# Kernel tuning notes

Hardware: AMD Instinct MI355X
Metric: run time of the kernel (lower is better)

Reference implementation:

```python
import jax, jax.numpy as jnp
import numpy as np

G = 3  # group_num
EPS = 1e-5


def _ln(x, g, b):
    m = x.mean(-1, keepdims=True)
    v = x.var(-1, keepdims=True)
    return (x - m) / jnp.sqrt(v + EPS) * g + b


def _gcm(x, w_qk, b_qk, ct_w1, ct_b1, ct_g, ct_be, ct_w2, ct_b2,
         lw_w1, lw_b1, lw_g, lw_be, lw_w2, lw_b2):
    # x: [B, 768, H, W] (pre-concatenated group feature)
    b, c, h, w = x.shape
    gc = c // G
    # channel shuffle: b (g c) h w -> b (c g) h w
    xs = x.reshape(b, G, gc, h, w).transpose(0, 2, 1, 3, 4).reshape(b, c, h, w)
    out = xs.reshape(b, G, gc, h, w)            # b g c h w
    value = out.reshape(b, G, gc, h * w)        # b g c n
    # fc_qk (Linear gc->1) over the channel axis, softmax over spatial n
    logits = jnp.einsum('bgcn,c->bgn', value, w_qk) + b_qk
    attn = jax.nn.softmax(logits, axis=-1)       # b g n
    context = jnp.einsum('bgcn,bgn->bgc', value, attn)  # b g c
    lvl_context = context.reshape(b, c)          # b (g c)
    # ctx_transform: Linear -> LN -> ReLU -> Linear
    h1 = jax.nn.relu(_ln(context @ ct_w1.T + ct_b1, ct_g, ct_be))
    ctx = h1 @ ct_w2.T + ct_b2                   # b g c
    # lvl_weight: Linear -> LN -> ReLU -> Linear -> Sigmoid
    l1 = jax.nn.relu(_ln(lvl_context @ lw_w1.T + lw_b1, lw_g, lw_be))
    lvlw = jax.nn.sigmoid(l1 @ lw_w2.T + lw_b2)  # b g (=3)
    ctx = ctx * lvlw[:, :, None]
    return (out + ctx[:, :, :, None, None]).sum(axis=1)  # b c_g h w


def setup_inputs() -> dict:
    key = jax.random.key(0)
    ks = jax.random.split(key, 16)
    B = 8
    sizes = [(128, 128), (64, 64), (32, 32), (16, 16)]
    inp = {}
    for i, (h, w) in enumerate(sizes):
        inp[f'g{i}'] = jax.random.normal(ks[i], (B, 768, h, w), jnp.float32)
    inp['x_last'] = jax.random.normal(ks[4], (B, 256, 8, 8), jnp.float32)
    s = 0.05
    inp['w_qk'] = jax.random.normal(ks[5], (4, 256), jnp.float32) * s
    inp['b_qk'] = jax.random.normal(ks[6], (4,), jnp.float32) * s
    inp['ct_w1'] = jax.random.normal(ks[7], (4, 64, 256), jnp.float32) * s
    inp['ct_b1'] = jax.random.normal(ks[8], (4, 64), jnp.float32) * s
    inp['ct_g'] = jnp.ones((4, 64), jnp.float32)
    inp['ct_be'] = jnp.zeros((4, 64), jnp.float32)
    inp['ct_w2'] = jax.random.normal(ks[9], (4, 256, 64), jnp.float32) * s
    inp['ct_b2'] = jax.random.normal(ks[10], (4, 256), jnp.float32) * s
    inp['lw_w1'] = jax.random.normal(ks[11], (4, 768, 768), jnp.float32) * s
    inp['lw_b1'] = jax.random.normal(ks[12], (4, 768), jnp.float32) * s
    inp['lw_g'] = jnp.ones((4, 768), jnp.float32)
    inp['lw_be'] = jnp.zeros((4, 768), jnp.float32)
    inp['lw_w2'] = jax.random.normal(ks[13], (4, 3, 768), jnp.float32) * s
    inp['lw_b2'] = jax.random.normal(ks[14], (4, 3), jnp.float32) * s
    return inp


def reference(g0, g1, g2, g3, x_last, w_qk, b_qk, ct_w1, ct_b1, ct_g, ct_be,
              ct_w2, ct_b2, lw_w1, lw_b1, lw_g, lw_be, lw_w2, lw_b2):
    outs = []
    for i, g in enumerate([g0, g1, g2, g3]):
        outs.append(_gcm(g, w_qk[i], b_qk[i], ct_w1[i], ct_b1[i], ct_g[i],
                         ct_be[i], ct_w2[i], ct_b2[i], lw_w1[i], lw_b1[i],
                         lw_g[i], lw_be[i], lw_w2[i], lw_b2[i]))
    return (*outs, x_last)
```

## Files before the change

### kernel.cpp

```cpp
#include <hip/hip_runtime.h>

#define NB 8
#define NWG 680
#define PSTRIDE 772

typedef float f4 __attribute__((ext_vector_type(4)));

__device__ __forceinline__ f4 ntload(const float* p) {
  return __builtin_nontemporal_load((const f4*)p);
}
__device__ __forceinline__ void ntstore(float* p, f4 v) {
  __builtin_nontemporal_store(v, (f4*)p);
}
__device__ __forceinline__ float hsum(f4 v) { return v.x + v.y + v.z + v.w; }

struct KFArgs {
  const float* x[4];
  float* outp[4];
  float* partial;
  int N[4];
};

__global__ __launch_bounds__(512, 2) void kf_fused(KFArgs a, const float* __restrict__ wqk_all) {
  __shared__ float red[2][768];
  __shared__ float zl[24];

  int wg = blockIdx.x;
  int lvl, b, idx;
  if (wg < 512)      { lvl = 0; b = wg >> 6;            idx = wg & 63; }
  else if (wg < 640) { int r = wg - 512; lvl = 1; b = r >> 4; idx = r & 15; }
  else if (wg < 672) { int r = wg - 640; lvl = 2; b = r >> 2; idx = r & 3; }
  else               { int r = wg - 672; lvl = 3; b = r;      idx = 0; }
  int N = a.N[lvl];
  int col0 = idx * 256;
  const float* __restrict__ xb = a.x[lvl] + (size_t)b * 768 * N;
  float* __restrict__ outb = a.outp[lvl] + (size_t)b * 256 * N;
  int tid = threadIdx.x;
  int snq = tid & 7, oq = tid >> 3, wv = tid >> 6;

  int srow[4][3];
  float wq[4];
#pragma unroll
  for (int j = 0; j < 4; ++j) {
    int c2 = oq + 64 * j;
    wq[j] = wqk_all[lvl * 256 + c2];
#pragma unroll
    for (int k = 0; k < 3; ++k) {
      int f = c2 + (k << 8);
      srow[j][k] = (f % 3) * 256 + f / 3;
    }
  }

  float acc[4][3] = {{0.f, 0.f, 0.f}, {0.f, 0.f, 0.f}, {0.f, 0.f, 0.f}, {0.f, 0.f, 0.f}};
  float za[3] = {0.f, 0.f, 0.f};

  f4 A[12], B[12];

  auto issue = [&](f4* buf, int tile) {
    int n0 = col0 + tile * 32 + snq * 4;
#pragma unroll
    for (int j = 0; j < 4; ++j)
#pragma unroll
      for (int k = 0; k < 3; ++k)
        buf[j * 3 + k] = ntload(xb + (size_t)srow[j][k] * N + n0);
  };

  auto body = [&](f4* cur, f4* nxt, int tt, bool pre) {
    int n0 = col0 + tt * 32 + snq * 4;
    if (pre) issue(nxt, tt + 1);
    f4 pg[3] = {{0.f, 0.f, 0.f, 0.f}, {0.f, 0.f, 0.f, 0.f}, {0.f, 0.f, 0.f, 0.f}};
#pragma unroll
    for (int j = 0; j < 4; ++j)
#pragma unroll
      for (int k = 0; k < 3; ++k)
        pg[k] += cur[j * 3 + k] * wq[j];
#pragma unroll
    for (int k = 0; k < 3; ++k) {
#pragma unroll
      for (int m = 8; m <= 32; m <<= 1) {
        pg[k].x += __shfl_xor(pg[k].x, m);
        pg[k].y += __shfl_xor(pg[k].y, m);
        pg[k].z += __shfl_xor(pg[k].z, m);
        pg[k].w += __shfl_xor(pg[k].w, m);
      }
    }
    float* rb = red[tt & 1];
    if ((tid & 63) < 8) {
#pragma unroll
      for (int k = 0; k < 3; ++k)
        *(f4*)(rb + (wv * 24 + k * 8 + snq) * 4) = pg[k];
    }
    asm volatile("s_waitcnt lgkmcnt(0)" ::: "memory");
    __builtin_amdgcn_sched_barrier(0);
    __builtin_amdgcn_s_barrier();
    __builtin_amdgcn_sched_barrier(0);
    f4 sev[3];
#pragma unroll
    for (int k = 0; k < 3; ++k) {
      f4 s = {0.f, 0.f, 0.f, 0.f};
#pragma unroll
      for (int w = 0; w < 8; ++w) s += *(const f4*)(rb + (w * 24 + k * 8 + snq) * 4);
      f4 e;
      e.x = __expf(s.x); e.y = __expf(s.y); e.z = __expf(s.z); e.w = __expf(s.w);
      sev[k] = e;
    }
    if (tid < 8) {
#pragma unroll
      for (int k = 0; k < 3; ++k) za[k] += hsum(sev[k]);
    }
#pragma unroll
    for (int j = 0; j < 4; ++j) {
      f4 ov = cur[j * 3 + 0] + cur[j * 3 + 1] + cur[j * 3 + 2];
      *(f4*)(outb + (size_t)(oq + 64 * j) * N + n0) = ov;
#pragma unroll
      for (int k = 0; k < 3; ++k)
        acc[j][k] += hsum(cur[j * 3 + k] * sev[k]);
    }
  };

  issue(A, 0);
  for (int tt = 0; tt < 8; tt += 2) {
    body(A, B, tt, true);
    body(B, A, tt + 1, tt + 1 < 7);
  }

  float* pw = a.partial + (size_t)wg * PSTRIDE;
#pragma unroll
  for (int j = 0; j < 4; ++j)
#pragma unroll
    for (int k = 0; k < 3; ++k) {
      float v = acc[j][k];
      v += __shfl_xor(v, 1);
      v += __shfl_xor(v, 2);
      v += __shfl_xor(v, 4);
      if (snq == 0) pw[k * 256 + oq + 64 * j] = v;
    }
  if (tid < 8) {
#pragma unroll
    for (int k = 0; k < 3; ++k) zl[tid * 3 + k] = za[k];
  }
  __syncthreads();
  if (tid < 3) {
    float z = 0.f;
#pragma unroll
    for (int s = 0; s < 8; ++s) z += zl[s * 3 + tid];
    pw[768 + tid] = z;
  }
}

__device__ __forceinline__ float blk_sum256(float v, float* sr4) {
  for (int o = 32; o; o >>= 1) v += __shfl_xor(v, o);
  __syncthreads();
  if ((threadIdx.x & 63) == 0) sr4[threadIdx.x >> 6] = v;
  __syncthreads();
  return sr4[0] + sr4[1] + sr4[2] + sr4[3];
}

__global__ __launch_bounds__(256) void k4_mlp(
    const float* __restrict__ partial,
    const float* __restrict__ ct_w1, const float* __restrict__ ct_b1,
    const float* __restrict__ ct_g,  const float* __restrict__ ct_be,
    const float* __restrict__ ct_w2, const float* __restrict__ ct_b2,
    const float* __restrict__ lw_w1, const float* __restrict__ lw_b1,
    const float* __restrict__ lw_g,  const float* __restrict__ lw_be,
    const float* __restrict__ lw_w2, const float* __restrict__ lw_b2,
    float* __restrict__ add_all) {
  int b = blockIdx.x, lvl = blockIdx.y;
  int t = threadIdx.x;
  static const int cnt_[4] = {64, 16, 4, 1};
  static const int base_[4] = {0, 512, 640, 672};
  int cnt = cnt_[lvl];
  int wg0 = base_[lvl] + b * cnt;

  const float* w1 = ct_w1 + lvl * 64 * 256;
  const float* b1 = ct_b1 + lvl * 64;
  const float* cg = ct_g + lvl * 64;
  const float* cbe = ct_be + lvl * 64;
  const float* w2 = ct_w2 + lvl * 256 * 64;
  const float* b2 = ct_b2 + lvl * 256;
  const float* W1 = lw_w1 + (size_t)lvl * 768 * 768;
  const float* B1 = lw_b1 + lvl * 768;
  const float* Lg = lw_g + lvl * 768;
  const float* Lbe = lw_be + lvl * 768;
  const float* W2 = lw_w2 + lvl * 3 * 768;
  const float* B2 = lw_b2 + lvl * 3;
  float* addp = add_all + ((size_t)lvl * NB + b) * 256;

  __shared__ float sctx[768];
  __shared__ float sh1[3][64];
  __shared__ float sl1[768];
  __shared__ float slvlw[3];
  __shared__ float sr4[4];
  __shared__ float sZ[3];

  float s0 = 0.f, s1 = 0.f, s2 = 0.f;
  for (int w = 0; w < cnt; ++w) {
    const float* pw = partial + (size_t)(wg0 + w) * PSTRIDE;
    s0 += pw[t];
    s1 += pw[t + 256];
    s2 += pw[t + 512];
  }
  if (t < 3) {
    float z = 0.f;
    for (int w = 0; w < cnt; ++w) z += partial[(size_t)(wg0 + w) * PSTRIDE + 768 + t];
    sZ[t] = z;
  }
  __syncthreads();
  sctx[t] = s0 / sZ[0];
  sctx[t + 256] = s1 / sZ[1];
  sctx[t + 512] = s2 / sZ[2];
  __syncthreads();

  if (t < 192) {
    int g = t >> 6, j = t & 63;
    const f4* w4 = (const f4*)(w1 + j * 256);
    const f4* c4 = (const f4*)(sctx + g * 256);
    f4 acc = {0.f, 0.f, 0.f, 0.f};
#pragma unroll 8
    for (int k = 0; k < 64; ++k) acc += c4[k] * w4[k];
    sh1[g][j] = hsum(acc) + b1[j];
  }
  __syncthreads();
  int wv = t >> 6, ln = t & 63;
  if (wv < 3) {
    float v = sh1[wv][ln];
    float s = v;
    for (int o = 32; o; o >>= 1) s += __shfl_xor(s, o);
    float mean = s * (1.f / 64.f);
    float d = v - mean;
    float q = d * d;
    for (int o = 32; o; o >>= 1) q += __shfl_xor(q, o);
    float var = q * (1.f / 64.f);
    float y = d * rsqrtf(var + 1e-5f) * cg[ln] + cbe[ln];
    sh1[wv][ln] = fmaxf(y, 0.f);
  }
  __syncthreads();
  float l1v[3];
#pragma unroll
  for (int r = 0; r < 3; ++r) {
    int j = t + r * 256;
    const f4* W4 = (const f4*)(W1 + (size_t)j * 768);
    const f4* s4 = (const f4*)sctx;
    f4 acc = {0.f, 0.f, 0.f, 0.f};
#pragma unroll 8
    for (int k = 0; k < 192; ++k) acc += s4[k] * W4[k];
    l1v[r] = hsum(acc) + B1[j];
  }
  float S = blk_sum256(l1v[0] + l1v[1] + l1v[2], sr4);
  float mean = S * (1.f / 768.f);
  float q = 0.f;
#pragma unroll
  for (int r = 0; r < 3; ++r) { float d = l1v[r] - mean; q += d * d; }
  float var = blk_sum256(q, sr4) * (1.f / 768.f);
  float inv = rsqrtf(var + 1e-5f);
#pragma unroll
  for (int r = 0; r < 3; ++r) {
    int j = t + r * 256;
    float y = (l1v[r] - mean) * inv * Lg[j] + Lbe[j];
    sl1[j] = fmaxf(y, 0.f);
  }
  __syncthreads();
  if (wv < 3) {
    float acc = 0.f;
    for (int j = ln; j < 768; j += 64) acc = fmaf(sl1[j], W2[wv * 768 + j], acc);
    for (int o = 32; o; o >>= 1) acc += __shfl_xor(acc, o);
    if (ln == 0) slvlw[wv] = 1.f / (1.f + __expf(-(acc + B2[wv])));
  }
  __syncthreads();
  {
    int c2 = t;
    float a = 0.f;
#pragma unroll
    for (int g = 0; g < 3; ++g) {
      const f4* w4 = (const f4*)(w2 + c2 * 64);
      const f4* h4 = (const f4*)(sh1[g]);
      f4 acc = {0.f, 0.f, 0.f, 0.f};
#pragma unroll
      for (int j = 0; j < 16; ++j) acc += h4[j] * w4[j];
      a += (hsum(acc) + b2[c2]) * slvlw[g];
    }
    addp[c2] = a;
  }
}

__global__ __launch_bounds__(256) void k5_add(float* __restrict__ out,
                                              const float* __restrict__ add_all,
                                              const float* __restrict__ xlast) {
  size_t f4i = (size_t)blockIdx.x * 256 + threadIdx.x;
  if (f4i >= 11141120) {
    size_t r = f4i - 11141120;
    f4 v = ntload(xlast + (r << 2));
    ntstore(out + (f4i << 2), v);
    return;
  }
  int lvl, lgN2;
  size_t base;
  if (f4i < 8388608)       { lvl = 0; base = 0;        lgN2 = 12; }
  else if (f4i < 10485760) { lvl = 1; base = 8388608;  lgN2 = 10; }
  else if (f4i < 11010048) { lvl = 2; base = 10485760; lgN2 = 8;  }
  else                     { lvl = 3; base = 11010048; lgN2 = 6;  }
  size_t lf4 = f4i - base;
  int bc = (int)(lf4 >> lgN2);
  float a = add_all[lvl * 2048 + bc];
  float* p = out + (f4i << 2);
  f4 v = *(const f4*)p;
  v += a;
  ntstore(p, v);
}

extern "C" void kernel_launch(void* const* d_in, const int* in_sizes, int n_in,
                              void* d_out, int out_size, void* d_ws, size_t ws_size,
                              hipStream_t stream) {
  const float* gx[4] = {(const float*)d_in[0], (const float*)d_in[1],
                        (const float*)d_in[2], (const float*)d_in[3]};
  const float* x_last = (const float*)d_in[4];
  const float* w_qk = (const float*)d_in[5];
  const float* ct_w1 = (const float*)d_in[7];
  const float* ct_b1 = (const float*)d_in[8];
  const float* ct_g  = (const float*)d_in[9];
  const float* ct_be = (const float*)d_in[10];
  const float* ct_w2 = (const float*)d_in[11];
  const float* ct_b2 = (const float*)d_in[12];
  const float* lw_w1 = (const float*)d_in[13];
  const float* lw_b1 = (const float*)d_in[14];
  const float* lw_g  = (const float*)d_in[15];
  const float* lw_be = (const float*)d_in[16];
  const float* lw_w2 = (const float*)d_in[17];
  const float* lw_b2 = (const float*)d_in[18];
  float* out = (float*)d_out;
  float* ws = (float*)d_ws;

  static const int Ns[4] = {16384, 4096, 1024, 256};
  static const size_t outOff[4] = {0, 33554432, 41943040, 44040192};

  float* partb = ws;
  float* addb  = ws + NWG * PSTRIDE;

  KFArgs af;
  for (int i = 0; i < 4; ++i) {
    af.x[i] = gx[i];
    af.outp[i] = out + outOff[i];
    af.N[i] = Ns[i];
  }
  af.partial = partb;

  kf_fused<<<dim3(NWG), dim3(512), 0, stream>>>(af, w_qk);
  k4_mlp<<<dim3(NB, 4), dim3(256), 0, stream>>>(partb, ct_w1, ct_b1, ct_g, ct_be,
                                                ct_w2, ct_b2, lw_w1, lw_b1, lw_g,
                                                lw_be, lw_w2, lw_b2, addb);
  k5_add<<<dim3(43648), dim3(256), 0, stream>>>(out, addb, x_last);
}
```

Baseline: 304.8 us.

## Split fused kernel into one workgroup per 32-column tile, drop software pipelining

Measured after the change: 316.2 us. +3.7%, slower.

```diff
diff --git a/kernel.cpp b/kernel.cpp
--- a/kernel.cpp
+++ b/kernel.cpp
@@ -1,7 +1,7 @@
 #include <hip/hip_runtime.h>
 
 #define NB 8
-#define NWG 680
+#define NTILE 5440
 #define PSTRIDE 772
 
 typedef float f4 __attribute__((ext_vector_type(4)));
@@ -21,22 +21,22 @@
   int N[4];
 };
 
-__global__ __launch_bounds__(512, 2) void kf_fused(KFArgs a, const float* __restrict__ wqk_all) {
-  __shared__ float red[2][768];
+__global__ __launch_bounds__(512, 4) void kf_fused(KFArgs a, const float* __restrict__ wqk_all) {
+  __shared__ float red[768];
   __shared__ float zl[24];
 
   int wg = blockIdx.x;
   int lvl, b, idx;
-  if (wg < 512)      { lvl = 0; b = wg >> 6;            idx = wg & 63; }
-  else if (wg < 640) { int r = wg - 512; lvl = 1; b = r >> 4; idx = r & 15; }
-  else if (wg < 672) { int r = wg - 640; lvl = 2; b = r >> 2; idx = r & 3; }
-  else               { int r = wg - 672; lvl = 3; b = r;      idx = 0; }
+  if (wg < 4096)      { lvl = 0; b = wg >> 9;            idx = wg & 511; }
+  else if (wg < 5120) { int r = wg - 4096; lvl = 1; b = r >> 7; idx = r & 127; }
+  else if (wg < 5376) { int r = wg - 5120; lvl = 2; b = r >> 5; idx = r & 31; }
+  else                { int r = wg - 5376; lvl = 3; b = r >> 3; idx = r & 7; }
   int N = a.N[lvl];
-  int col0 = idx * 256;
   const float* __restrict__ xb = a.x[lvl] + (size_t)b * 768 * N;
   float* __restrict__ outb = a.outp[lvl] + (size_t)b * 256 * N;
   int tid = threadIdx.x;
   int snq = tid & 7, oq = tid >> 3, wv = tid >> 6;
+  int n0 = idx * 32 + snq * 4;
 
   int srow[4][3];
   float wq[4];
@@ -51,77 +51,62 @@
     }
   }
 
-  float acc[4][3] = {{0.f, 0.f, 0.f}, {0.f, 0.f, 0.f}, {0.f, 0.f, 0.f}, {0.f, 0.f, 0.f}};
-  float za[3] = {0.f, 0.f, 0.f};
-
-  f4 A[12], B[12];
-
-  auto issue = [&](f4* buf, int tile) {
-    int n0 = col0 + tile * 32 + snq * 4;
-#pragma unroll
-    for (int j = 0; j < 4; ++j)
-#pragma unroll
-      for (int k = 0; k < 3; ++k)
-        buf[j * 3 + k] = ntload(xb + (size_t)srow[j][k] * N + n0);
-  };
-
-  auto body = [&](f4* cur, f4* nxt, int tt, bool pre) {
-    int n0 = col0 + tt * 32 + snq * 4;
-    if (pre) issue(nxt, tt + 1);
-    f4 pg[3] = {{0.f, 0.f, 0.f, 0.f}, {0.f, 0.f, 0.f, 0.f}, {0.f, 0.f, 0.f, 0.f}};
-#pragma unroll
-    for (int j = 0; j < 4; ++j)
-#pragma unroll
-      for (int k = 0; k < 3; ++k)
-        pg[k] += cur[j * 3 + k] * wq[j];
-#pragma unroll
-    for (int k = 0; k < 3; ++k) {
-#pragma unroll
-      for (int m = 8; m <= 32; m <<= 1) {
-        pg[k].x += __shfl_xor(pg[k].x, m);
-        pg[k].y += __shfl_xor(pg[k].y, m);
-        pg[k].z += __shfl_xor(pg[k].z, m);
-        pg[k].w += __shfl_xor(pg[k].w, m);
-      }
+  f4 X[12];
+#pragma unroll
+  for (int j = 0; j < 4; ++j)
+#pragma unroll
+    for (int k = 0; k < 3; ++k)
+      X[j * 3 + k] = ntload(xb + (size_t)srow[j][k] * N + n0);
+
+  f4 pg[3] = {{0.f, 0.f, 0.f, 0.f}, {0.f, 0.f, 0.f, 0.f}, {0.f, 0.f, 0.f, 0.f}};
+#pragma unroll
+  for (int j = 0; j < 4; ++j)
+#pragma unroll
+    for (int k = 0; k < 3; ++k)
+      pg[k] += X[j * 3 + k] * wq[j];
+#pragma unroll
+  for (int k = 0; k < 3; ++k) {
+#pragma unroll
+    for (int m = 8; m <= 32; m <<= 1) {
+      pg[k].x += __shfl_xor(pg[k].x, m);
+      pg[k].y += __shfl_xor(pg[k].y, m);
+      pg[k].z += __shfl_xor(pg[k].z, m);
+      pg[k].w += __shfl_xor(pg[k].w, m);
     }
-    float* rb = red[tt & 1];
-    if ((tid & 63) < 8) {
-#pragma unroll
-      for (int k = 0; k < 3; ++k)
-        *(f4*)(rb + (wv * 24 + k * 8 + snq) * 4) = pg[k];
-    }
-    asm volatile("s_waitcnt lgkmcnt(0)" ::: "memory");
-    __builtin_amdgcn_sched_barrier(0);
-    __builtin_amdgcn_s_barrier();
-    __builtin_amdgcn_sched_barrier(0);
-    f4 sev[3];
-#pragma unroll
-    for (int k = 0; k < 3; ++k) {
-      f4 s = {0.f, 0.f, 0.f, 0.f};
-#pragma unroll
-      for (int w = 0; w < 8; ++w) s += *(const f4*)(rb + (w * 24 + k * 8 + snq) * 4);
-      f4 e;
-      e.x = __expf(s.x); e.y = __expf(s.y); e.z = __expf(s.z); e.w = __expf(s.w);
-      sev[k] = e;
-    }
-    if (tid < 8) {
-#pragma unroll
-      for (int k = 0; k < 3; ++k) za[k] += hsum(sev[k]);
-    }
-#pragma unroll
-    for (int j = 0; j < 4; ++j) {
-      f4 ov = cur[j * 3 + 0] + cur[j * 3 + 1] + cur[j * 3 + 2];
-      *(f4*)(outb + (size_t)(oq + 64 * j) * N + n0) = ov;
-#pragma unroll
-      for (int k = 0; k < 3; ++k)
-        acc[j][k] += hsum(cur[j * 3 + k] * sev[k]);
-    }
-  };
-
-  issue(A, 0);
-  for (int tt = 0; tt < 8; tt += 2) {
-    body(A, B, tt, true);
-    body(B, A, tt + 1, tt + 1 < 7);
+  }
+  if ((tid & 63) < 8) {
+#pragma unroll
+    for (int k = 0; k < 3; ++k)
+      *(f4*)(red + (wv * 24 + k * 8 + snq) * 4) = pg[k];
+  }
+  asm volatile("s_waitcnt lgkmcnt(0)" ::: "memory");
+  __builtin_amdgcn_sched_barrier(0);
+  __builtin_amdgcn_s_barrier();
+  __builtin_amdgcn_sched_barrier(0);
+
+  f4 sev[3];
+#pragma unroll
+  for (int k = 0; k < 3; ++k) {
+    f4 s = {0.f, 0.f, 0.f, 0.f};
+#pragma unroll
+    for (int w = 0; w < 8; ++w) s += *(const f4*)(red + (w * 24 + k * 8 + snq) * 4);
+    f4 e;
+    e.x = __expf(s.x); e.y = __expf(s.y); e.z = __expf(s.z); e.w = __expf(s.w);
+    sev[k] = e;
+  }
+  if (tid < 8) {
+#pragma unroll
+    for (int k = 0; k < 3; ++k) zl[tid * 3 + k] = hsum(sev[k]);
+  }
+
+  float acc[4][3];
+#pragma unroll
+  for (int j = 0; j < 4; ++j) {
+    f4 ov = X[j * 3 + 0] + X[j * 3 + 1] + X[j * 3 + 2];
+    *(f4*)(outb + (size_t)(oq + 64 * j) * N + n0) = ov;
+#pragma unroll
+    for (int k = 0; k < 3; ++k)
+      acc[j][k] = hsum(X[j * 3 + k] * sev[k]);
   }
 
   float* pw = a.partial + (size_t)wg * PSTRIDE;
@@ -135,10 +120,6 @@
       v += __shfl_xor(v, 4);
       if (snq == 0) pw[k * 256 + oq + 64 * j] = v;
     }
-  if (tid < 8) {
-#pragma unroll
-    for (int k = 0; k < 3; ++k) zl[tid * 3 + k] = za[k];
-  }
   __syncthreads();
   if (tid < 3) {
     float z = 0.f;
@@ -167,8 +148,8 @@
     float* __restrict__ add_all) {
   int b = blockIdx.x, lvl = blockIdx.y;
   int t = threadIdx.x;
-  static const int cnt_[4] = {64, 16, 4, 1};
-  static const int base_[4] = {0, 512, 640, 672};
+  static const int cnt_[4] = {512, 128, 32, 8};
+  static const int base_[4] = {0, 4096, 5120, 5376};
   int cnt = cnt_[lvl];
   int wg0 = base_[lvl] + b * cnt;
 
@@ -192,17 +173,28 @@
   __shared__ float slvlw[3];
   __shared__ float sr4[4];
   __shared__ float sZ[3];
-
+  __shared__ float zp[96];
+
+  if (t < 96) {
+    int g = t >> 5, j = t & 31;
+    float z = 0.f;
+    for (int w = j; w < cnt; w += 32)
+      z += partial[(size_t)(wg0 + w) * PSTRIDE + 768 + g];
+    zp[t] = z;
+  }
   float s0 = 0.f, s1 = 0.f, s2 = 0.f;
+#pragma unroll 8
   for (int w = 0; w < cnt; ++w) {
     const float* pw = partial + (size_t)(wg0 + w) * PSTRIDE;
     s0 += pw[t];
     s1 += pw[t + 256];
     s2 += pw[t + 512];
   }
+  __syncthreads();
   if (t < 3) {
     float z = 0.f;
-    for (int w = 0; w < cnt; ++w) z += partial[(size_t)(wg0 + w) * PSTRIDE + 768 + t];
+#pragma unroll
+    for (int i = 0; i < 32; ++i) z += zp[t * 32 + i];
     sZ[t] = z;
   }
   __syncthreads();
@@ -334,7 +326,7 @@
   static const size_t outOff[4] = {0, 33554432, 41943040, 44040192};
 
   float* partb = ws;
-  float* addb  = ws + NWG * PSTRIDE;
+  float* addb  = ws + (size_t)NTILE * PSTRIDE;
 
   KFArgs af;
   for (int i = 0; i < 4; ++i) {
@@ -344,7 +336,7 @@
   }
   af.partial = partb;
 
-  kf_fused<<<dim3(NWG), dim3(512), 0, stream>>>(af, w_qk);
+  kf_fused<<<dim3(NTILE), dim3(512), 0, stream>>>(af, w_qk);
   k4_mlp<<<dim3(NB, 4), dim3(256), 0, stream>>>(partb, ct_w1, ct_b1, ct_g, ct_be,
                                                 ct_w2, ct_b2, lw_w1, lw_b1, lw_g,
                                                 lw_be, lw_w2, lw_b2, addb);
```
